# Kernel optimization log

Hardware: AMD Instinct MI355X
Metric: run time of the kernel (lower is better)

## Reference

```python
import jax, jax.numpy as jnp
import numpy as np

BATCH = 2
L = 2048
D_MODEL = 1024
D_STATE = 16
D_CONV = 4
EXPAND = 2
D_INNER = EXPAND * D_MODEL  # 2048
DT_RANK = (D_MODEL + 15) // 16  # 64


def setup_inputs() -> dict:
    key = jax.random.key(0)
    ks = jax.random.split(key, 12)
    f = jnp.float32
    hidden_states = jax.random.normal(ks[0], (BATCH, L, D_MODEL), f)
    input2 = jax.random.normal(ks[1], (BATCH, L, D_MODEL), f)
    in_proj1_w = jax.random.normal(ks[2], (D_INNER, D_MODEL), f) * (D_MODEL ** -0.5)
    in_proj2_w = jax.random.normal(ks[3], (D_INNER, D_MODEL), f) * (D_MODEL ** -0.5)
    conv_w = jax.random.normal(ks[4], (D_INNER, 1, D_CONV), f) * (D_CONV ** -0.5)
    conv_b = jax.random.normal(ks[5], (D_INNER,), f) * 0.02
    x_proj_w = jax.random.normal(ks[6], (DT_RANK + 2 * D_STATE, D_INNER), f) * (D_INNER ** -0.5)
    dt_std = DT_RANK ** -0.5
    dt_proj_w = jax.random.uniform(ks[7], (D_INNER, DT_RANK), f, -dt_std, dt_std)
    # dt bias init: inverse softplus of log-uniform dt in [1e-3, 1e-1]
    dt = jnp.exp(jax.random.uniform(ks[8], (D_INNER,), f) * (np.log(0.1) - np.log(0.001)) + np.log(0.001))
    dt = jnp.clip(dt, 1e-4, None)
    dt_proj_b = dt + jnp.log(-jnp.expm1(-dt))
    # A_log init: log(1..d_state) broadcast over channels
    A_log = jnp.log(jnp.broadcast_to(jnp.arange(1, D_STATE + 1, dtype=f), (D_INNER, D_STATE)))
    D = jnp.ones((D_INNER,), f)
    out_proj_w = jax.random.normal(ks[9], (D_MODEL, D_INNER), f) * (D_INNER ** -0.5)
    return dict(hidden_states=hidden_states, input2=input2, in_proj1_w=in_proj1_w,
                in_proj2_w=in_proj2_w, conv_w=conv_w, conv_b=conv_b, x_proj_w=x_proj_w,
                dt_proj_w=dt_proj_w, dt_proj_b=dt_proj_b, A_log=A_log, D=D,
                out_proj_w=out_proj_w)


def _forward(hidden_states, input2, in_proj1_w, in_proj2_w, conv_w, conv_b,
             x_proj_w, dt_proj_w, dt_proj_b, A_log, D, out_proj_w):
    # in_proj: (B,L,Dm) -> (B,d_inner,L)
    x = jnp.einsum('bld,ed->bel', hidden_states, in_proj1_w)
    z = jnp.einsum('bld,ed->bel', input2, in_proj2_w)
    # causal depthwise conv1d (left pad d_conv-1, equiv to torch pad+truncate) + SiLU
    xc = jax.lax.conv_general_dilated(x, conv_w, (1,), [(D_CONV - 1, 0)],
                                      dimension_numbers=('NCH', 'OIH', 'NCH'),
                                      feature_group_count=D_INNER)
    x = jax.nn.silu(xc + conv_b[None, :, None])
    # x_proj -> dt, B, C
    x_dbl = jnp.einsum('bel,re->brl', x, x_proj_w)  # (B, dt_rank+2n, L)
    dt = x_dbl[:, :DT_RANK]
    Bm = x_dbl[:, DT_RANK:DT_RANK + D_STATE]       # (B, n, L)
    Cm = x_dbl[:, DT_RANK + D_STATE:]               # (B, n, L)
    delta = jnp.einsum('brl,er->bel', dt, dt_proj_w)
    delta = jax.nn.softplus(delta + dt_proj_b[None, :, None])  # (B, d_inner, L)
    A = -jnp.exp(A_log)  # (d_inner, n)
    # selective scan over time (time-major for lax.scan)
    dlt = jnp.transpose(delta, (2, 0, 1))  # (L, B, d)
    u = jnp.transpose(x, (2, 0, 1))        # (L, B, d)
    Bt = jnp.transpose(Bm, (2, 0, 1))      # (L, B, n)
    Ct = jnp.transpose(Cm, (2, 0, 1))      # (L, B, n)

    def step(state, inp):
        d_t, u_t, B_t, C_t = inp
        dA = jnp.exp(d_t[..., None] * A)                        # (B, d, n)
        state = state * dA + (d_t * u_t)[..., None] * B_t[:, None, :]
        y_t = jnp.einsum('bdn,bn->bd', state, C_t)
        return state, y_t

    init = jnp.zeros((hidden_states.shape[0], D_INNER, D_STATE), x.dtype)
    _, ys = jax.lax.scan(step, init, (dlt, u, Bt, Ct))
    y = jnp.transpose(ys, (1, 2, 0)) + D[None, :, None] * x  # (B, d, L)
    y = y * jax.nn.silu(z)
    out = jnp.einsum('bel,de->bld', y, out_proj_w)  # out_proj, no bias
    return out


def reference(hidden_states, input2, in_proj1_w, in_proj2_w, conv_w, conv_b,
              x_proj_w, dt_proj_w, dt_proj_b, A_log, D, out_proj_w):
    return _forward(hidden_states, input2, in_proj1_w, in_proj2_w, conv_w, conv_b,
                    x_proj_w, dt_proj_w, dt_proj_b, A_log, D, out_proj_w)
```

## Files before the change

kernel.cpp:

```cpp
#include <hip/hip_runtime.h>
#include <cstddef>
#include <cmath>
#include <type_traits>

#define BATCH 2
#define LSEQ 2048
#define DM 1024
#define DSTATE 16
#define DI 2048
#define DTR 64
#define XDR 96
#define NC 64
#define TC 32
#define PN (4096 * 96)

using f32x4 = __attribute__((ext_vector_type(4))) float;
using bf16x8 = __attribute__((ext_vector_type(8))) short;

__device__ __forceinline__ unsigned short f2bf(float f) {
  union { float f; unsigned int u; } c; c.f = f;
  unsigned int u = c.u;
  return (unsigned short)((u + 0x7FFFu + ((u >> 16) & 1u)) >> 16);
}
__device__ __forceinline__ float bf2f(unsigned short h) {
  union { unsigned int u; float f; } c; c.u = ((unsigned int)h) << 16;
  return c.f;
}
__device__ __forceinline__ unsigned int pack2(float a, float b) {
  return (unsigned int)f2bf(a) | ((unsigned int)f2bf(b) << 16);
}

__device__ __forceinline__ void gl_lds16(const void* g, void* l) {
  __builtin_amdgcn_global_load_lds(
      (const __attribute__((address_space(1))) void*)g,
      (__attribute__((address_space(3))) void*)l, 16, 0, 0);
}

__device__ __forceinline__ float softplus_fast(float x) {
  float ex = __expf(x);
  return (x > 20.f) ? x : __logf(1.f + ex);
}

__device__ __forceinline__ void pow_tree(float q1, float* dA) {
  float q2 = q1 * q1;
  float q3 = q2 * q1;
  float q4 = q2 * q2;
  float q8 = q4 * q4;
  float q5 = q4 * q1, q6 = q4 * q2, q7 = q4 * q3;
  dA[0] = q1;  dA[1] = q2;  dA[2] = q3;  dA[3] = q4;
  dA[4] = q5;  dA[5] = q6;  dA[6] = q7;  dA[7] = q8;
  dA[8] = q8 * q1;  dA[9] = q8 * q2;  dA[10] = q8 * q3;  dA[11] = q8 * q4;
  dA[12] = q8 * q5; dA[13] = q8 * q6; dA[14] = q8 * q7;  dA[15] = q8 * q8;
}

__global__ __launch_bounds__(256) void cvt_bf16_kernel(
    const float* __restrict__ s, unsigned short* __restrict__ d, int n8) {
  int i = blockIdx.x * 256 + threadIdx.x;
  if (i >= n8) return;
  const float4* sp = reinterpret_cast<const float4*>(s) + (size_t)i * 2;
  float4 a = sp[0], b = sp[1];
  uint4 v = make_uint4(pack2(a.x, a.y), pack2(a.z, a.w), pack2(b.x, b.y),
                       pack2(b.z, b.w));
  *(reinterpret_cast<uint4*>(d) + i) = v;
}

__global__ __launch_bounds__(256) void cvt2_bf16_kernel(
    const float* __restrict__ s1, unsigned short* __restrict__ d1,
    const float* __restrict__ s2, unsigned short* __restrict__ d2, int n8) {
  int i = blockIdx.x * 256 + threadIdx.x;
  const float* s;
  unsigned short* d;
  int k;
  if (i < n8) {
    s = s1; d = d1; k = i;
  } else {
    s = s2; d = d2; k = i - n8;
    if (k >= n8) return;
  }
  const float4* sp = reinterpret_cast<const float4*>(s) + (size_t)k * 2;
  float4 a = sp[0], b = sp[1];
  uint4 v = make_uint4(pack2(a.x, a.y), pack2(a.z, a.w), pack2(b.x, b.y),
                       pack2(b.z, b.w));
  *(reinterpret_cast<uint4*>(d) + k) = v;
}

template <typename OutT>
__global__ __launch_bounds__(256) void gemm_bf16_t(
    const unsigned short* __restrict__ A, const unsigned short* __restrict__ B,
    OutT* __restrict__ C, int K, int lda, int ldb, int ldc) {
  __shared__ __align__(16) unsigned short As[128][64];
  __shared__ __align__(16) unsigned short Bs[128][64];

  const int tid = threadIdx.x;
  const int lane = tid & 63;
  const int w = tid >> 6;

  const int gx = gridDim.x;
  const int nwg = gx * gridDim.y;
  const int id = blockIdx.y * gx + blockIdx.x;
  const int cpx = nwg >> 3;
  const int lt = (id & 7) * cpx + (id >> 3);
  const size_t m0 = (size_t)(lt / gx) * 128;
  const size_t n0 = (size_t)(lt % gx) * 128;

  const int rsub = lane >> 3;
  const int sslot = (lane & 7) ^ rsub;
  const unsigned short* Ab = A + m0 * lda + (size_t)rsub * lda + sslot * 8;
  const unsigned short* Bb = B + n0 * ldb + (size_t)rsub * ldb + sslot * 8;

  f32x4 acc[4][4] = {};

  const int fr = lane & 15;
  const int q = lane >> 4;
  const int f7 = fr & 7;

  for (int k0 = 0; k0 < K; k0 += 64) {
#pragma unroll
    for (int i = 0; i < 4; ++i) {
      const int r0 = w * 32 + i * 8;
      gl_lds16(Ab + (size_t)r0 * lda + k0, &As[r0][0]);
      gl_lds16(Bb + (size_t)r0 * ldb + k0, &Bs[r0][0]);
    }
    __syncthreads();

    bf16x8 af[4][2], bf_[4][2];
#pragma unroll
    for (int i = 0; i < 4; ++i) {
#pragma unroll
      for (int kk = 0; kk < 2; ++kk) {
        const int sA = (((kk * 4 + q) ^ f7) << 3);
        af[i][kk] = *reinterpret_cast<const bf16x8*>(
            &As[(w >> 1) * 64 + i * 16 + fr][sA]);
        bf_[i][kk] = *reinterpret_cast<const bf16x8*>(
            &Bs[(w & 1) * 64 + i * 16 + fr][sA]);
      }
    }
#pragma unroll
    for (int kk = 0; kk < 2; ++kk)
#pragma unroll
      for (int i = 0; i < 4; ++i)
#pragma unroll
        for (int j = 0; j < 4; ++j)
          acc[i][j] = __builtin_amdgcn_mfma_f32_16x16x32_bf16(
              af[i][kk], bf_[j][kk], acc[i][j], 0, 0, 0);
    __syncthreads();
  }

  const int crb = q * 4;
#pragma unroll
  for (int i = 0; i < 4; ++i) {
    size_t row = m0 + (w >> 1) * 64 + i * 16 + crb;
#pragma unroll
    for (int j = 0; j < 4; ++j) {
      size_t col = n0 + (w & 1) * 64 + j * 16 + fr;
#pragma unroll
      for (int r = 0; r < 4; ++r) {
        if constexpr (std::is_same_v<OutT, unsigned short>)
          C[(row + r) * ldc + col] = f2bf(acc[i][j][r]);
        else
          C[(row + r) * ldc + col] = acc[i][j][r];
      }
    }
  }
}

__global__ __launch_bounds__(256) void gemm_delta(
    const unsigned short* __restrict__ A, const unsigned short* __restrict__ B,
    const float* __restrict__ bias, unsigned short* __restrict__ C, int K,
    int lda, int ldb, int ldc) {
  __shared__ __align__(16) unsigned short As[128][64];
  __shared__ __align__(16) unsigned short Bs[128][64];

  const int tid = threadIdx.x;
  const int lane = tid & 63;
  const int w = tid >> 6;

  const int gx = gridDim.x;
  const int nwg = gx * gridDim.y;
  const int id = blockIdx.y * gx + blockIdx.x;
  const int cpx = nwg >> 3;
  const int lt = (id & 7) * cpx + (id >> 3);
  const size_t m0 = (size_t)(lt / gx) * 128;
  const size_t n0 = (size_t)(lt % gx) * 128;

  const int rsub = lane >> 3;
  const int sslot = (lane & 7) ^ rsub;
  const unsigned short* Ab = A + m0 * lda + (size_t)rsub * lda + sslot * 8;
  const unsigned short* Bb = B + n0 * ldb + (size_t)rsub * ldb + sslot * 8;

  f32x4 acc[4][4] = {};

  const int fr = lane & 15;
  const int q = lane >> 4;
  const int f7 = fr & 7;

  for (int k0 = 0; k0 < K; k0 += 64) {
#pragma unroll
    for (int i = 0; i < 4; ++i) {
      const int r0 = w * 32 + i * 8;
      gl_lds16(Ab + (size_t)r0 * lda + k0, &As[r0][0]);
      gl_lds16(Bb + (size_t)r0 * ldb + k0, &Bs[r0][0]);
    }
    __syncthreads();

    bf16x8 af[4][2], bf_[4][2];
#pragma unroll
    for (int i = 0; i < 4; ++i) {
#pragma unroll
      for (int kk = 0; kk < 2; ++kk) {
        const int sA = (((kk * 4 + q) ^ f7) << 3);
        af[i][kk] = *reinterpret_cast<const bf16x8*>(
            &As[(w >> 1) * 64 + i * 16 + fr][sA]);
        bf_[i][kk] = *reinterpret_cast<const bf16x8*>(
            &Bs[(w & 1) * 64 + i * 16 + fr][sA]);
      }
    }
#pragma unroll
    for (int kk = 0; kk < 2; ++kk)
#pragma unroll
      for (int i = 0; i < 4; ++i)
#pragma unroll
        for (int j = 0; j < 4; ++j)
          acc[i][j] = __builtin_amdgcn_mfma_f32_16x16x32_bf16(
              af[i][kk], bf_[j][kk], acc[i][j], 0, 0, 0);
    __syncthreads();
  }

  const int crb = q * 4;
#pragma unroll
  for (int i = 0; i < 4; ++i) {
    size_t row = m0 + (w >> 1) * 64 + i * 16 + crb;
#pragma unroll
    for (int j = 0; j < 4; ++j) {
      size_t col = n0 + (w & 1) * 64 + j * 16 + fr;
      float bv = bias[col];
#pragma unroll
      for (int r = 0; r < 4; ++r)
        C[(row + r) * ldc + col] = f2bf(softplus_fast(acc[i][j][r] + bv));
    }
  }
}

__global__ __launch_bounds__(256) void gemm_xdbl(
    const unsigned short* __restrict__ A,
    const unsigned short* __restrict__ B,
    float* __restrict__ P) {
  __shared__ __align__(16) unsigned short As[128][64];
  __shared__ __align__(16) unsigned short Bs[96][64];

  const int tid = threadIdx.x;
  const int lane = tid & 63;
  const int w = tid >> 6;
  const size_t m0 = (size_t)blockIdx.x * 128;
  const int k0base = blockIdx.y * 512;

  const int rsub = lane >> 3;
  const int sslot = (lane & 7) ^ rsub;
  const unsigned short* Ab = A + m0 * DI + (size_t)rsub * DI + sslot * 8;
  const unsigned short* Bb = B + (size_t)rsub * DI + sslot * 8;

  f32x4 acc[4][3] = {};

  const int fr = lane & 15;
  const int q = lane >> 4;
  const int f7 = fr & 7;

  for (int ks = 0; ks < 8; ++ks) {
    const int k0 = k0base + ks * 64;
#pragma unroll
    for (int i = 0; i < 4; ++i) {
      const int r0 = w * 32 + i * 8;
      gl_lds16(Ab + (size_t)r0 * DI + k0, &As[r0][0]);
    }
#pragma unroll
    for (int i = 0; i < 3; ++i) {
      const int r0 = w * 24 + i * 8;
      gl_lds16(Bb + (size_t)r0 * DI + k0, &Bs[r0][0]);
    }
    __syncthreads();

    bf16x8 af[4][2], bf_[3][2];
#pragma unroll
    for (int kk = 0; kk < 2; ++kk) {
      const int sA = (((kk * 4 + q) ^ f7) << 3);
#pragma unroll
      for (int i = 0; i < 4; ++i)
        af[i][kk] = *reinterpret_cast<const bf16x8*>(
            &As[(w >> 1) * 64 + i * 16 + fr][sA]);
#pragma unroll
      for (int j = 0; j < 3; ++j)
        bf_[j][kk] = *reinterpret_cast<const bf16x8*>(
            &Bs[(w & 1) * 48 + j * 16 + fr][sA]);
    }
#pragma unroll
    for (int kk = 0; kk < 2; ++kk)
#pragma unroll
      for (int i = 0; i < 4; ++i)
#pragma unroll
        for (int j = 0; j < 3; ++j)
          acc[i][j] = __builtin_amdgcn_mfma_f32_16x16x32_bf16(
              af[i][kk], bf_[j][kk], acc[i][j], 0, 0, 0);
    __syncthreads();
  }

  float* Pz = P + (size_t)blockIdx.y * PN;
  const int crb = q * 4;
#pragma unroll
  for (int i = 0; i < 4; ++i) {
    size_t row = m0 + (w >> 1) * 64 + i * 16 + crb;
#pragma unroll
    for (int j = 0; j < 3; ++j) {
      int col = (w & 1) * 48 + j * 16 + fr;
#pragma unroll
      for (int r = 0; r < 4; ++r) Pz[(row + r) * XDR + col] = acc[i][j][r];
    }
  }
}

__global__ __launch_bounds__(256) void reduce4x_kernel(
    const float* __restrict__ P, unsigned short* __restrict__ dtB,
    float* __restrict__ BC) {
  int i = blockIdx.x * 256 + threadIdx.x;
  int row = i / XDR, col = i - row * XDR;
  float s = (P[i] + P[PN + i]) + (P[2 * PN + i] + P[3 * PN + i]);
  if (col < 64)
    dtB[row * 64 + col] = f2bf(s);
  else
    BC[row * 32 + (col - 64)] = s;
}

__global__ __launch_bounds__(256) void conv_silu_kernel(
    const unsigned short* __restrict__ x, const float* __restrict__ w,
    const float* __restrict__ cb, unsigned short* __restrict__ out) {
  int idx = blockIdx.x * 256 + threadIdx.x;
  int e4 = idx % (DI / 4);
  int bl = idx / (DI / 4);
  int l = bl % LSEQ;
  int e = e4 * 4;

  const float4* cw = reinterpret_cast<const float4*>(w);
  float4 w0 = cw[e], w1 = cw[e + 1], w2 = cw[e + 2], w3 = cw[e + 3];
  float4 acc = *reinterpret_cast<const float4*>(&cb[e]);

#define TAPK(K, COMP)                                                       \
  {                                                                         \
    int ls = l - 3 + (K);                                                   \
    if (ls >= 0) {                                                          \
      uint2 xv = *reinterpret_cast<const uint2*>(                           \
          &x[((size_t)(bl) - 3 + (K)) * DI + e]);                           \
      acc.x = fmaf(bf2f((unsigned short)(xv.x & 0xffff)), w0.COMP, acc.x);  \
      acc.y = fmaf(bf2f((unsigned short)(xv.x >> 16)), w1.COMP, acc.y);     \
      acc.z = fmaf(bf2f((unsigned short)(xv.y & 0xffff)), w2.COMP, acc.z);  \
      acc.w = fmaf(bf2f((unsigned short)(xv.y >> 16)), w3.COMP, acc.w);     \
    }                                                                       \
  }
  TAPK(0, x)
  TAPK(1, y)
  TAPK(2, z)
  TAPK(3, w)
#undef TAPK

  acc.x = acc.x / (1.f + expf(-acc.x));
  acc.y = acc.y / (1.f + expf(-acc.y));
  acc.z = acc.z / (1.f + expf(-acc.z));
  acc.w = acc.w / (1.f + expf(-acc.w));
  *reinterpret_cast<uint2*>(&out[(size_t)bl * DI + e]) =
      make_uint2(pack2(acc.x, acc.y), pack2(acc.z, acc.w));
}

__global__ __launch_bounds__(256) void scan_passA(
    const unsigned short* __restrict__ dB, const unsigned short* __restrict__ u,
    const float* __restrict__ bc, const float* __restrict__ A_log,
    float* __restrict__ sEnd, float* __restrict__ sProd) {
  int g = blockIdx.x * 256 + threadIdx.x;
  int e = g & (DI - 1);
  int c = (g >> 11) & (NC - 1);
  int b = g >> 17;

  const float nA0 = -__expf(A_log[e * DSTATE]);
  bool aok = true;
#pragma unroll
  for (int n = 1; n < DSTATE; ++n) {
    float nAn = -__expf(A_log[e * DSTATE + n]);
    aok = aok && (fabsf(nAn - (float)(n + 1) * nA0) <= 1e-4f * fabsf(nAn));
  }

  const size_t off = ((size_t)b * LSEQ + c * TC) * DI + e;
  const size_t boff0 = ((size_t)b * LSEQ + c * TC) * 32;

  float s[DSTATE], P[DSTATE];
#pragma unroll
  for (int n = 0; n < DSTATE; ++n) { s[n] = 0.f; P[n] = 1.f; }

  unsigned short dq[4], uq[4];
#pragma unroll
  for (int j = 0; j < 4; ++j) {
    size_t o = off + (size_t)j * DI;
    dq[j] = dB[o];
    uq[j] = u[o];
  }

  for (int tb = 0; tb < TC; tb += 4) {
#pragma unroll
    for (int j = 0; j < 4; ++j) {
      const int t = tb + j;
      float d = bf2f(dq[j]);
      float ut = bf2f(uq[j]);
      if (t + 4 < TC) {
        size_t o = off + (size_t)(t + 4) * DI;
        dq[j] = dB[o];
        uq[j] = u[o];
      }
      float db = d * ut;
      float dA[DSTATE];
      if (aok) {
        pow_tree(__expf(d * nA0), dA);
      } else {
#pragma unroll
        for (int n = 0; n < DSTATE; ++n)
          dA[n] = __expf(-d * __expf(A_log[e * DSTATE + n]));
      }
      const float4* bcp =
          reinterpret_cast<const float4*>(&bc[boff0 + (size_t)t * 32]);
      float4 B0 = bcp[0], B1 = bcp[1], B2 = bcp[2], B3 = bcp[3];
      float Bv[DSTATE] = {B0.x, B0.y, B0.z, B0.w, B1.x, B1.y, B1.z, B1.w,
                          B2.x, B2.y, B2.z, B2.w, B3.x, B3.y, B3.z, B3.w};
#pragma unroll
      for (int n = 0; n < DSTATE; ++n) {
        s[n] = fmaf(s[n], dA[n], db * Bv[n]);
        P[n] *= dA[n];
      }
    }
  }

  size_t o = (((size_t)b * NC + c) * DI + e) * DSTATE;
  float4* se = reinterpret_cast<float4*>(&sEnd[o]);
  float4* sp = reinterpret_cast<float4*>(&sProd[o]);
  se[0] = make_float4(s[0], s[1], s[2], s[3]);
  se[1] = make_float4(s[4], s[5], s[6], s[7]);
  se[2] = make_float4(s[8], s[9], s[10], s[11]);
  se[3] = make_float4(s[12], s[13], s[14], s[15]);
  sp[0] = make_float4(P[0], P[1], P[2], P[3]);
  sp[1] = make_float4(P[4], P[5], P[6], P[7]);
  sp[2] = make_float4(P[8], P[9], P[10], P[11]);
  sp[3] = make_float4(P[12], P[13], P[14], P[15]);
}

__global__ __launch_bounds__(256) void scan_passB(
    float* __restrict__ sEnd, const float* __restrict__ sProd) {
  int g = blockIdx.x * 256 + threadIdx.x;
  int n = g & 15;
  int e = (g >> 4) & (DI - 1);
  int b = g >> 15;
  float s = 0.f;
  for (int c = 0; c < NC; ++c) {
    size_t o = (((size_t)b * NC + c) * DI + e) * DSTATE + n;
    float se = sEnd[o];
    float sp = sProd[o];
    sEnd[o] = s;
    s = fmaf(s, sp, se);
  }
}

__global__ __launch_bounds__(256) void scan_passC(
    const unsigned short* __restrict__ dB, const unsigned short* __restrict__ u,
    const unsigned short* __restrict__ z, const float* __restrict__ bc,
    const float* __restrict__ A_log, const float* __restrict__ Dv,
    const float* __restrict__ sInit, unsigned short* __restrict__ gOut) {
  int g = blockIdx.x * 256 + threadIdx.x;
  int e = g & (DI - 1);
  int c = (g >> 11) & (NC - 1);
  int b = g >> 17;

  const float nA0 = -__expf(A_log[e * DSTATE]);
  bool aok = true;
#pragma unroll
  for (int n = 1; n < DSTATE; ++n) {
    float nAn = -__expf(A_log[e * DSTATE + n]);
    aok = aok && (fabsf(nAn - (float)(n + 1) * nA0) <= 1e-4f * fabsf(nAn));
  }
  const float Dval = Dv[e];

  const size_t off = ((size_t)b * LSEQ + c * TC) * DI + e;
  const size_t boff0 = ((size_t)b * LSEQ + c * TC) * 32;

  float s[DSTATE];
  {
    size_t o = (((size_t)b * NC + c) * DI + e) * DSTATE;
    const float4* si = reinterpret_cast<const float4*>(&sInit[o]);
    float4 s0 = si[0], s1 = si[1], s2 = si[2], s3 = si[3];
    s[0] = s0.x; s[1] = s0.y; s[2] = s0.z; s[3] = s0.w;
    s[4] = s1.x; s[5] = s1.y; s[6] = s1.z; s[7] = s1.w;
    s[8] = s2.x; s[9] = s2.y; s[10] = s2.z; s[11] = s2.w;
    s[12] = s3.x; s[13] = s3.y; s[14] = s3.z; s[15] = s3.w;
  }

  unsigned short dq[4], uq[4], zq[4];
#pragma unroll
  for (int j = 0; j < 4; ++j) {
    size_t o = off + (size_t)j * DI;
    dq[j] = dB[o];
    uq[j] = u[o];
    zq[j] = z[o];
  }

  for (int tb = 0; tb < TC; tb += 4) {
#pragma unroll
    for (int j = 0; j < 4; ++j) {
      const int t = tb + j;
      float d = bf2f(dq[j]);
      float ut = bf2f(uq[j]);
      float zt = bf2f(zq[j]);
      if (t + 4 < TC) {
        size_t o = off + (size_t)(t + 4) * DI;
        dq[j] = dB[o];
        uq[j] = u[o];
        zq[j] = z[o];
      }
      float db = d * ut;
      float dA[DSTATE];
      if (aok) {
        pow_tree(__expf(d * nA0), dA);
      } else {
#pragma unroll
        for (int n = 0; n < DSTATE; ++n)
          dA[n] = __expf(-d * __expf(A_log[e * DSTATE + n]));
      }
      const float4* bcp =
          reinterpret_cast<const float4*>(&bc[boff0 + (size_t)t * 32]);
      float4 B0 = bcp[0], B1 = bcp[1], B2 = bcp[2], B3 = bcp[3];
      float4 C0 = bcp[4], C1 = bcp[5], C2 = bcp[6], C3 = bcp[7];
      float Bv[DSTATE] = {B0.x, B0.y, B0.z, B0.w, B1.x, B1.y, B1.z, B1.w,
                          B2.x, B2.y, B2.z, B2.w, B3.x, B3.y, B3.z, B3.w};
      float Cv[DSTATE] = {C0.x, C0.y, C0.z, C0.w, C1.x, C1.y, C1.z, C1.w,
                          C2.x, C2.y, C2.z, C2.w, C3.x, C3.y, C3.z, C3.w};
      float y0 = 0.f, y1 = 0.f, y2 = 0.f, y3 = 0.f;
#pragma unroll
      for (int n = 0; n < 4; ++n) {
        s[n] = fmaf(s[n], dA[n], db * Bv[n]);
        y0 = fmaf(s[n], Cv[n], y0);
        s[n + 4] = fmaf(s[n + 4], dA[n + 4], db * Bv[n + 4]);
        y1 = fmaf(s[n + 4], Cv[n + 4], y1);
        s[n + 8] = fmaf(s[n + 8], dA[n + 8], db * Bv[n + 8]);
        y2 = fmaf(s[n + 8], Cv[n + 8], y2);
        s[n + 12] = fmaf(s[n + 12], dA[n + 12], db * Bv[n + 12]);
        y3 = fmaf(s[n + 12], Cv[n + 12], y3);
      }
      float y = (y0 + y1) + (y2 + y3);
      float gate = zt / (1.f + __expf(-zt));
      gOut[off + (size_t)t * DI] = f2bf((y + Dval * ut) * gate);
    }
  }
}

extern "C" void kernel_launch(void* const* d_in, const int* in_sizes, int n_in,
                              void* d_out, int out_size, void* d_ws,
                              size_t ws_size, hipStream_t stream) {
  const float* hs = (const float*)d_in[0];
  const float* in2 = (const float*)d_in[1];
  const float* w1 = (const float*)d_in[2];
  const float* w2 = (const float*)d_in[3];
  const float* cw = (const float*)d_in[4];
  const float* cb = (const float*)d_in[5];
  const float* xpw = (const float*)d_in[6];
  const float* dtw = (const float*)d_in[7];
  const float* dtb = (const float*)d_in[8];
  const float* alog = (const float*)d_in[9];
  const float* Dv = (const float*)d_in[10];
  const float* ow = (const float*)d_in[11];
  float* out = (float*)d_out;

  const size_t BLE = (size_t)BATCH * LSEQ * DI;
  const size_t BLM = (size_t)BATCH * LSEQ * DM;
  const size_t WN = (size_t)DI * DM;
  const size_t SC = (size_t)BATCH * NC * DI * DSTATE;

  float* W = (float*)d_ws;
  float* bufX = W;
  float* M2 = W + BLE;
  float* M3 = M2 + BLE / 2;
  float* M4 = M3 + BLE / 2;
  float* sEnd = M4 + BLE / 2;
  float* sProd = sEnd + SC;
  float* BC = sProd + SC;

  unsigned short* hsb = (unsigned short*)M2;
  unsigned short* zb = (unsigned short*)M2;
  unsigned short* in2b = (unsigned short*)M3;
  unsigned short* ub = (unsigned short*)M3;
  unsigned short* wb1 = (unsigned short*)M4;
  unsigned short* wb2 = wb1 + WN;
  float* xdblP = M4;
  unsigned short* xpwB = (unsigned short*)(M4 + 4 * PN);
  unsigned short* dtB = (unsigned short*)(M4 + 4 * PN + 98304 + 16);
  unsigned short* dtwB = (unsigned short*)(M4 + 4 * PN + 98304 + 131072 + 32);
  unsigned short* bufG = (unsigned short*)M4;
  unsigned short* xpreB = (unsigned short*)bufX;
  unsigned short* dB = (unsigned short*)bufX;
  unsigned short* owb = (unsigned short*)sProd;

  const int M = BATCH * LSEQ;
  dim3 blk(256);

  cvt2_bf16_kernel<<<(int)(2 * (BLM / 8) / 256), blk, 0, stream>>>(
      hs, hsb, in2, in2b, (int)(BLM / 8));
  cvt2_bf16_kernel<<<(int)(2 * (WN / 8) / 256), blk, 0, stream>>>(
      w1, wb1, w2, wb2, (int)(WN / 8));
  gemm_bf16_t<unsigned short><<<dim3(DI / 128, M / 128), blk, 0, stream>>>(
      hsb, wb1, xpreB, DM, DM, DM, DI);
  gemm_bf16_t<unsigned short><<<dim3(DI / 128, M / 128), blk, 0, stream>>>(
      in2b, wb2, zb, DM, DM, DM, DI);
  conv_silu_kernel<<<(M * (DI / 4)) / 256, blk, 0, stream>>>(xpreB, cw, cb,
                                                             ub);
  cvt_bf16_kernel<<<96, blk, 0, stream>>>(xpw, xpwB, XDR * DI / 8);
  cvt_bf16_kernel<<<64, blk, 0, stream>>>(dtw, dtwB, DI * DTR / 8);
  gemm_xdbl<<<dim3(M / 128, 4), blk, 0, stream>>>(ub, xpwB, xdblP);
  reduce4x_kernel<<<(M * XDR) / 256, blk, 0, stream>>>(xdblP, dtB, BC);
  gemm_delta<<<dim3(DI / 128, M / 128), blk, 0, stream>>>(
      dtB, dtwB, dtb, dB, DTR, DTR, DTR, DI);
  scan_passA<<<(BATCH * DI * NC) / 256, blk, 0, stream>>>(dB, ub, BC, alog,
                                                          sEnd, sProd);
  scan_passB<<<(BATCH * DI * DSTATE) / 256, blk, 0, stream>>>(sEnd, sProd);
  cvt_bf16_kernel<<<(int)(WN / 8 / 256), blk, 0, stream>>>(ow, owb,
                                                           (int)(WN / 8));
  scan_passC<<<(BATCH * DI * NC) / 256, blk, 0, stream>>>(
      dB, ub, zb, BC, alog, Dv, sEnd, bufG);
  gemm_bf16_t<float><<<dim3(DM / 128, M / 128), blk, 0, stream>>>(
      bufG, owb, out, DI, DI, DI, DM);
}
```

Before: 265.1 us.

## Store delta, z and u in chunk-major transposed layout for vectorized scan loads

The delta and z GEMM epilogues now write bf16 outputs in a (batch, chunk, channel, time) layout, and a new kernel transposes u the same way. The scan passes can then load 8 time steps per thread as one 16-byte vector instead of doing strided 2-byte loads. The chunk count is halved and the chunk length doubled (NC 32, TC 64), which means fewer chunk states to combine but less thread parallelism in the scan. Workspace buffers are reassigned to fit the new arrays. The cost is one extra transpose kernel, and each vector load now touches addresses 128 bytes apart per lane.

```diff
diff --git a/kernel.cpp b/kernel.cpp
--- a/kernel.cpp
+++ b/kernel.cpp
@@ -10,12 +10,13 @@
 #define DI 2048
 #define DTR 64
 #define XDR 96
-#define NC 64
-#define TC 32
+#define NC 32
+#define TC 64
 #define PN (4096 * 96)
 
 using f32x4 = __attribute__((ext_vector_type(4))) float;
 using bf16x8 = __attribute__((ext_vector_type(8))) short;
+using u16x8 = __attribute__((ext_vector_type(8))) unsigned short;
 
 __device__ __forceinline__ unsigned short f2bf(float f) {
   union { float f; unsigned int u; } c; c.f = f;
@@ -51,6 +52,14 @@
   dA[4] = q5;  dA[5] = q6;  dA[6] = q7;  dA[7] = q8;
   dA[8] = q8 * q1;  dA[9] = q8 * q2;  dA[10] = q8 * q3;  dA[11] = q8 * q4;
   dA[12] = q8 * q5; dA[13] = q8 * q6; dA[14] = q8 * q7;  dA[15] = q8 * q8;
+}
+
+__device__ __forceinline__ size_t xaddr(int row, int col) {
+  int b_ = row >> 11;
+  int lloc = row & (LSEQ - 1);
+  int c_ = lloc >> 6;
+  int t0 = lloc & (TC - 1);
+  return (((size_t)b_ * NC + c_) * DI + col) * TC + t0;
 }
 
 __global__ __launch_bounds__(256) void cvt_bf16_kernel(
@@ -84,7 +93,7 @@
   *(reinterpret_cast<uint4*>(d) + k) = v;
 }
 
-template <typename OutT>
+template <typename OutT, bool XPOSE>
 __global__ __launch_bounds__(256) void gemm_bf16_t(
     const unsigned short* __restrict__ A, const unsigned short* __restrict__ B,
     OutT* __restrict__ C, int K, int lda, int ldb, int ldc) {
@@ -149,16 +158,23 @@
   const int crb = q * 4;
 #pragma unroll
   for (int i = 0; i < 4; ++i) {
-    size_t row = m0 + (w >> 1) * 64 + i * 16 + crb;
+    int row = (int)m0 + (w >> 1) * 64 + i * 16 + crb;
 #pragma unroll
     for (int j = 0; j < 4; ++j) {
-      size_t col = n0 + (w & 1) * 64 + j * 16 + fr;
-#pragma unroll
-      for (int r = 0; r < 4; ++r) {
-        if constexpr (std::is_same_v<OutT, unsigned short>)
-          C[(row + r) * ldc + col] = f2bf(acc[i][j][r]);
-        else
-          C[(row + r) * ldc + col] = acc[i][j][r];
+      int col = (int)n0 + (w & 1) * 64 + j * 16 + fr;
+      if constexpr (XPOSE) {
+        size_t base = xaddr(row, col);
+        *reinterpret_cast<uint2*>(&C[base]) =
+            make_uint2(pack2(acc[i][j][0], acc[i][j][1]),
+                       pack2(acc[i][j][2], acc[i][j][3]));
+      } else {
+#pragma unroll
+        for (int r = 0; r < 4; ++r) {
+          if constexpr (std::is_same_v<OutT, unsigned short>)
+            C[(size_t)(row + r) * ldc + col] = f2bf(acc[i][j][r]);
+          else
+            C[(size_t)(row + r) * ldc + col] = acc[i][j][r];
+        }
       }
     }
   }
@@ -167,7 +183,7 @@
 __global__ __launch_bounds__(256) void gemm_delta(
     const unsigned short* __restrict__ A, const unsigned short* __restrict__ B,
     const float* __restrict__ bias, unsigned short* __restrict__ C, int K,
-    int lda, int ldb, int ldc) {
+    int lda, int ldb) {
   __shared__ __align__(16) unsigned short As[128][64];
   __shared__ __align__(16) unsigned short Bs[128][64];
 
@@ -229,14 +245,17 @@
   const int crb = q * 4;
 #pragma unroll
   for (int i = 0; i < 4; ++i) {
-    size_t row = m0 + (w >> 1) * 64 + i * 16 + crb;
+    int row = (int)m0 + (w >> 1) * 64 + i * 16 + crb;
 #pragma unroll
     for (int j = 0; j < 4; ++j) {
-      size_t col = n0 + (w & 1) * 64 + j * 16 + fr;
+      int col = (int)n0 + (w & 1) * 64 + j * 16 + fr;
       float bv = bias[col];
-#pragma unroll
-      for (int r = 0; r < 4; ++r)
-        C[(row + r) * ldc + col] = f2bf(softplus_fast(acc[i][j][r] + bv));
+      float v0 = softplus_fast(acc[i][j][0] + bv);
+      float v1 = softplus_fast(acc[i][j][1] + bv);
+      float v2 = softplus_fast(acc[i][j][2] + bv);
+      float v3 = softplus_fast(acc[i][j][3] + bv);
+      *reinterpret_cast<uint2*>(&C[xaddr(row, col)]) =
+          make_uint2(pack2(v0, v1), pack2(v2, v3));
     }
   }
 }
@@ -368,14 +387,43 @@
       make_uint2(pack2(acc.x, acc.y), pack2(acc.z, acc.w));
 }
 
+__global__ __launch_bounds__(256) void xpose_u_kernel(
+    const unsigned short* __restrict__ u, unsigned short* __restrict__ uT) {
+  __shared__ unsigned short T[TC][256];
+  const int tid = threadIdx.x;
+  const int blk = blockIdx.x;
+  const int eb = blk & 7;
+  const int c = (blk >> 3) & (NC - 1);
+  const int b = blk >> 8;
+  const int e0 = eb * 256;
+
+  size_t rbase = ((size_t)b * LSEQ + (size_t)c * TC) * DI + e0 + tid;
+  for (int t = 0; t < TC; ++t) T[t][tid] = u[rbase + (size_t)t * DI];
+  __syncthreads();
+
+  size_t obase = (((size_t)b * NC + c) * DI + (e0 + tid)) * TC;
+#pragma unroll
+  for (int tb = 0; tb < TC; tb += 8) {
+    unsigned int w0 = (unsigned int)T[tb + 0][tid] |
+                      ((unsigned int)T[tb + 1][tid] << 16);
+    unsigned int w1 = (unsigned int)T[tb + 2][tid] |
+                      ((unsigned int)T[tb + 3][tid] << 16);
+    unsigned int w2 = (unsigned int)T[tb + 4][tid] |
+                      ((unsigned int)T[tb + 5][tid] << 16);
+    unsigned int w3 = (unsigned int)T[tb + 6][tid] |
+                      ((unsigned int)T[tb + 7][tid] << 16);
+    *reinterpret_cast<uint4*>(&uT[obase + tb]) = make_uint4(w0, w1, w2, w3);
+  }
+}
+
 __global__ __launch_bounds__(256) void scan_passA(
-    const unsigned short* __restrict__ dB, const unsigned short* __restrict__ u,
+    const unsigned short* __restrict__ dT, const unsigned short* __restrict__ uT,
     const float* __restrict__ bc, const float* __restrict__ A_log,
     float* __restrict__ sEnd, float* __restrict__ sProd) {
   int g = blockIdx.x * 256 + threadIdx.x;
   int e = g & (DI - 1);
   int c = (g >> 11) & (NC - 1);
-  int b = g >> 17;
+  int b = g >> 16;
 
   const float nA0 = -__expf(A_log[e * DSTATE]);
   bool aok = true;
@@ -385,32 +433,21 @@
     aok = aok && (fabsf(nAn - (float)(n + 1) * nA0) <= 1e-4f * fabsf(nAn));
   }
 
-  const size_t off = ((size_t)b * LSEQ + c * TC) * DI + e;
-  const size_t boff0 = ((size_t)b * LSEQ + c * TC) * 32;
+  const size_t sbase = (((size_t)b * NC + c) * DI + e) * TC;
+  const size_t boff0 = ((size_t)b * LSEQ + (size_t)c * TC) * 32;
 
   float s[DSTATE], P[DSTATE];
 #pragma unroll
   for (int n = 0; n < DSTATE; ++n) { s[n] = 0.f; P[n] = 1.f; }
 
-  unsigned short dq[4], uq[4];
-#pragma unroll
-  for (int j = 0; j < 4; ++j) {
-    size_t o = off + (size_t)j * DI;
-    dq[j] = dB[o];
-    uq[j] = u[o];
-  }
-
-  for (int tb = 0; tb < TC; tb += 4) {
-#pragma unroll
-    for (int j = 0; j < 4; ++j) {
+  for (int tb = 0; tb < TC; tb += 8) {
+    u16x8 dv = *reinterpret_cast<const u16x8*>(&dT[sbase + tb]);
+    u16x8 uv = *reinterpret_cast<const u16x8*>(&uT[sbase + tb]);
+#pragma unroll
+    for (int j = 0; j < 8; ++j) {
       const int t = tb + j;
-      float d = bf2f(dq[j]);
-      float ut = bf2f(uq[j]);
-      if (t + 4 < TC) {
-        size_t o = off + (size_t)(t + 4) * DI;
-        dq[j] = dB[o];
-        uq[j] = u[o];
-      }
+      float d = bf2f(dv[j]);
+      float ut = bf2f(uv[j]);
       float db = d * ut;
       float dA[DSTATE];
       if (aok) {
@@ -463,14 +500,14 @@
 }
 
 __global__ __launch_bounds__(256) void scan_passC(
-    const unsigned short* __restrict__ dB, const unsigned short* __restrict__ u,
-    const unsigned short* __restrict__ z, const float* __restrict__ bc,
+    const unsigned short* __restrict__ dT, const unsigned short* __restrict__ uT,
+    const unsigned short* __restrict__ zT, const float* __restrict__ bc,
     const float* __restrict__ A_log, const float* __restrict__ Dv,
     const float* __restrict__ sInit, unsigned short* __restrict__ gOut) {
   int g = blockIdx.x * 256 + threadIdx.x;
   int e = g & (DI - 1);
   int c = (g >> 11) & (NC - 1);
-  int b = g >> 17;
+  int b = g >> 16;
 
   const float nA0 = -__expf(A_log[e * DSTATE]);
   bool aok = true;
@@ -481,8 +518,9 @@
   }
   const float Dval = Dv[e];
 
-  const size_t off = ((size_t)b * LSEQ + c * TC) * DI + e;
-  const size_t boff0 = ((size_t)b * LSEQ + c * TC) * 32;
+  const size_t sbase = (((size_t)b * NC + c) * DI + e) * TC;
+  const size_t boff0 = ((size_t)b * LSEQ + (size_t)c * TC) * 32;
+  const size_t goff = ((size_t)b * LSEQ + (size_t)c * TC) * DI + e;
 
   float s[DSTATE];
   {
@@ -495,28 +533,16 @@
     s[12] = s3.x; s[13] = s3.y; s[14] = s3.z; s[15] = s3.w;
   }
 
-  unsigned short dq[4], uq[4], zq[4];
-#pragma unroll
-  for (int j = 0; j < 4; ++j) {
-    size_t o = off + (size_t)j * DI;
-    dq[j] = dB[o];
-    uq[j] = u[o];
-    zq[j] = z[o];
-  }
-
-  for (int tb = 0; tb < TC; tb += 4) {
-#pragma unroll
-    for (int j = 0; j < 4; ++j) {
+  for (int tb = 0; tb < TC; tb += 8) {
+    u16x8 dv = *reinterpret_cast<const u16x8*>(&dT[sbase + tb]);
+    u16x8 uv = *reinterpret_cast<const u16x8*>(&uT[sbase + tb]);
+    u16x8 zv = *reinterpret_cast<const u16x8*>(&zT[sbase + tb]);
+#pragma unroll
+    for (int j = 0; j < 8; ++j) {
       const int t = tb + j;
-      float d = bf2f(dq[j]);
-      float ut = bf2f(uq[j]);
-      float zt = bf2f(zq[j]);
-      if (t + 4 < TC) {
-        size_t o = off + (size_t)(t + 4) * DI;
-        dq[j] = dB[o];
-        uq[j] = u[o];
-        zq[j] = z[o];
-      }
+      float d = bf2f(dv[j]);
+      float ut = bf2f(uv[j]);
+      float zt = bf2f(zv[j]);
       float db = d * ut;
       float dA[DSTATE];
       if (aok) {
@@ -548,7 +574,7 @@
       }
       float y = (y0 + y1) + (y2 + y3);
       float gate = zt / (1.f + __expf(-zt));
-      gOut[off + (size_t)t * DI] = f2bf((y + Dval * ut) * gate);
+      gOut[goff + (size_t)t * DI] = f2bf((y + Dval * ut) * gate);
     }
   }
 }
@@ -576,7 +602,7 @@
   const size_t SC = (size_t)BATCH * NC * DI * DSTATE;
 
   float* W = (float*)d_ws;
-  float* bufX = W;
+  float* R0 = W;
   float* M2 = W + BLE;
   float* M3 = M2 + BLE / 2;
   float* M4 = M3 + BLE / 2;
@@ -584,19 +610,20 @@
   float* sProd = sEnd + SC;
   float* BC = sProd + SC;
 
+  unsigned short* xpreB = (unsigned short*)R0;
+  unsigned short* dT = (unsigned short*)R0;
+  unsigned short* bufG = (unsigned short*)(R0 + BLE / 2);
   unsigned short* hsb = (unsigned short*)M2;
-  unsigned short* zb = (unsigned short*)M2;
+  unsigned short* zT = (unsigned short*)M2;
   unsigned short* in2b = (unsigned short*)M3;
   unsigned short* ub = (unsigned short*)M3;
   unsigned short* wb1 = (unsigned short*)M4;
   unsigned short* wb2 = wb1 + WN;
-  float* xdblP = M4;
-  unsigned short* xpwB = (unsigned short*)(M4 + 4 * PN);
-  unsigned short* dtB = (unsigned short*)(M4 + 4 * PN + 98304 + 16);
-  unsigned short* dtwB = (unsigned short*)(M4 + 4 * PN + 98304 + 131072 + 32);
-  unsigned short* bufG = (unsigned short*)M4;
-  unsigned short* xpreB = (unsigned short*)bufX;
-  unsigned short* dB = (unsigned short*)bufX;
+  unsigned short* uT = (unsigned short*)M4;
+  float* xdblP = sProd;
+  unsigned short* xpwB = (unsigned short*)(sProd + 4 * PN);
+  unsigned short* dtB = (unsigned short*)(sProd + 4 * PN + 49152 + 16);
+  unsigned short* dtwB = (unsigned short*)(sProd + 4 * PN + 49152 + 131072 + 32);
   unsigned short* owb = (unsigned short*)sProd;
 
   const int M = BATCH * LSEQ;
@@ -606,25 +633,28 @@
       hs, hsb, in2, in2b, (int)(BLM / 8));
   cvt2_bf16_kernel<<<(int)(2 * (WN / 8) / 256), blk, 0, stream>>>(
       w1, wb1, w2, wb2, (int)(WN / 8));
-  gemm_bf16_t<unsigned short><<<dim3(DI / 128, M / 128), blk, 0, stream>>>(
-      hsb, wb1, xpreB, DM, DM, DM, DI);
-  gemm_bf16_t<unsigned short><<<dim3(DI / 128, M / 128), blk, 0, stream>>>(
-      in2b, wb2, zb, DM, DM, DM, DI);
+  gemm_bf16_t<unsigned short, false>
+      <<<dim3(DI / 128, M / 128), blk, 0, stream>>>(hsb, wb1, xpreB, DM, DM,
+                                                    DM, DI);
+  gemm_bf16_t<unsigned short, true>
+      <<<dim3(DI / 128, M / 128), blk, 0, stream>>>(in2b, wb2, zT, DM, DM, DM,
+                                                    0);
   conv_silu_kernel<<<(M * (DI / 4)) / 256, blk, 0, stream>>>(xpreB, cw, cb,
                                                              ub);
   cvt_bf16_kernel<<<96, blk, 0, stream>>>(xpw, xpwB, XDR * DI / 8);
   cvt_bf16_kernel<<<64, blk, 0, stream>>>(dtw, dtwB, DI * DTR / 8);
   gemm_xdbl<<<dim3(M / 128, 4), blk, 0, stream>>>(ub, xpwB, xdblP);
   reduce4x_kernel<<<(M * XDR) / 256, blk, 0, stream>>>(xdblP, dtB, BC);
-  gemm_delta<<<dim3(DI / 128, M / 128), blk, 0, stream>>>(
-      dtB, dtwB, dtb, dB, DTR, DTR, DTR, DI);
-  scan_passA<<<(BATCH * DI * NC) / 256, blk, 0, stream>>>(dB, ub, BC, alog,
+  gemm_delta<<<dim3(DI / 128, M / 128), blk, 0, stream>>>(dtB, dtwB, dtb, dT,
+                                                          DTR, DTR, DTR);
+  xpose_u_kernel<<<BATCH * NC * 8, blk, 0, stream>>>(ub, uT);
+  scan_passA<<<(BATCH * NC * DI) / 256, blk, 0, stream>>>(dT, uT, BC, alog,
                                                           sEnd, sProd);
   scan_passB<<<(BATCH * DI * DSTATE) / 256, blk, 0, stream>>>(sEnd, sProd);
   cvt_bf16_kernel<<<(int)(WN / 8 / 256), blk, 0, stream>>>(ow, owb,
                                                            (int)(WN / 8));
-  scan_passC<<<(BATCH * DI * NC) / 256, blk, 0, stream>>>(
-      dB, ub, zb, BC, alog, Dv, sEnd, bufG);
-  gemm_bf16_t<float><<<dim3(DM / 128, M / 128), blk, 0, stream>>>(
+  scan_passC<<<(BATCH * NC * DI) / 256, blk, 0, stream>>>(
+      dT, uT, zT, BC, alog, Dv, sEnd, bufG);
+  gemm_bf16_t<float, false><<<dim3(DM / 128, M / 128), blk, 0, stream>>>(
       bufG, owb, out, DI, DI, DI, DM);
 }
```

Result: slower. 294.4 us (+11.1%).
